# Optimization experiments

Hardware: AMD Instinct MI355X
Metric: run time of the kernel (lower is better)

Reference implementation:

```python
import jax, jax.numpy as jnp
from jax import lax
import numpy as np

B, N, C = 16, 4096, 81          # batch, rois, classes (incl. background)
VARIANCES = np.array([0.1, 0.1, 0.2, 0.2], dtype=np.float32)
MAX_TOTAL = 200                  # max_total_size (= per-class cap here)
K = 200                          # per-class candidates kept before NMS
SCORE_TH = 0.5
IOU_TH = 0.5                     # tf combined NMS default
EPS = 1e-8


def setup_inputs() -> dict:
    key = jax.random.key(0)
    k1, k2, k3, k4 = jax.random.split(key, 4)
    yx = jax.random.uniform(k1, (B, N, 2)) * 0.8
    hw = 0.05 + jax.random.uniform(k2, (B, N, 2)) * 0.15
    roi_bboxes = jnp.concatenate([yx, yx + hw], axis=-1)          # [B,N,4] y1x1y2x2 in [0,1]
    pred_deltas = jax.random.normal(k3, (B, N, C * 4)) * 0.5      # [B,N,C*4]
    logits = jax.random.normal(k4, (B, N, C)) * 3.0
    pred_label_probs = jax.nn.softmax(logits, axis=-1)            # [B,N,C]
    return {"roi_bboxes": roi_bboxes, "pred_deltas": pred_deltas,
            "pred_label_probs": pred_label_probs}


def delta_to_bbox(anchors, deltas):
    # anchors [...,4] y1,x1,y2,x2 ; deltas [...,4] dy,dx,dh,dw
    ah = anchors[..., 2] - anchors[..., 0]
    aw = anchors[..., 3] - anchors[..., 1]
    acy = anchors[..., 0] + 0.5 * ah
    acx = anchors[..., 1] + 0.5 * aw
    bh = jnp.exp(deltas[..., 2]) * ah
    bw = jnp.exp(deltas[..., 3]) * aw
    bcy = deltas[..., 0] * ah + acy
    bcx = deltas[..., 1] * aw + acx
    y1 = bcy - 0.5 * bh
    x1 = bcx - 0.5 * bw
    return jnp.stack([y1, x1, y1 + bh, x1 + bw], axis=-1)


def pairwise_iou(boxes):  # [K,4] -> [K,K]
    y1 = jnp.maximum(boxes[:, None, 0], boxes[None, :, 0])
    x1 = jnp.maximum(boxes[:, None, 1], boxes[None, :, 1])
    y2 = jnp.minimum(boxes[:, None, 2], boxes[None, :, 2])
    x2 = jnp.minimum(boxes[:, None, 3], boxes[None, :, 3])
    inter = jnp.maximum(y2 - y1, 0.0) * jnp.maximum(x2 - x1, 0.0)
    area = jnp.maximum(boxes[:, 2] - boxes[:, 0], 0.0) * jnp.maximum(boxes[:, 3] - boxes[:, 1], 0.0)
    union = area[:, None] + area[None, :] - inter
    return inter / (union + EPS)


def _nms_keep(boxes_k, scores_k):
    # boxes_k [K,4] sorted by score desc; greedy suppression mask
    ious = pairwise_iou(boxes_k)
    rng = jnp.arange(K)
    valid = scores_k > SCORE_TH

    def step(keep, i):
        sup = (ious[i] > IOU_TH) & (rng > i) & keep[i]
        return keep & ~sup, None

    keep, _ = lax.scan(step, valid, rng)
    return keep


def _per_class(boxes_c, scores_c):
    # boxes_c [N,4], scores_c [N] -> top-K candidates + NMS-kept scores
    sc, idx = lax.top_k(scores_c, K)
    bx = boxes_c[idx]                       # [K,4]
    keep = _nms_keep(bx, sc)
    return bx, jnp.where(keep, sc, 0.0)


def _per_image(boxes_b, scores_b):
    # boxes_b [N,C,4], scores_b [N,C]
    bx, sc = jax.vmap(_per_class, in_axes=(1, 1))(boxes_b, scores_b)  # [C,K,4],[C,K]
    top_sc, top_idx = lax.top_k(sc.reshape(-1), MAX_TOTAL)
    top_bx = bx.reshape(-1, 4)[top_idx]
    top_lbl = (top_idx // K).astype(jnp.float32)
    valid = top_sc > 0.0
    top_bx = jnp.clip(jnp.where(valid[:, None], top_bx, 0.0), 0.0, 1.0)  # clip_boxes=True
    return top_bx, jnp.where(valid, top_sc, 0.0), jnp.where(valid, top_lbl, 0.0)


def reference(roi_bboxes, pred_deltas, pred_label_probs):
    b, n, _ = roi_bboxes.shape
    c = pred_label_probs.shape[-1]
    deltas = pred_deltas.reshape(b, n, c, 4) * jnp.asarray(VARIANCES)
    pred_bboxes = delta_to_bbox(roi_bboxes[:, :, None, :], deltas)       # [B,N,C,4]
    bg = jnp.argmax(pred_label_probs, axis=-1) == 0                      # background mask
    scores = jnp.where(bg[..., None], 0.0, pred_label_probs)             # [B,N,C]
    final_bboxes, final_scores, final_labels = jax.vmap(_per_image)(pred_bboxes, scores)
    return final_bboxes, final_labels, final_scores
```

## Files before the change

kernel.cpp:

```cpp
#include <hip/hip_runtime.h>
#include <math.h>

#pragma clang fp contract(off)

constexpr int NB  = 16;
constexpr int NR  = 4096;
constexpr int NC  = 81;
constexpr int KK  = 200;
constexpr int CAP = 4096;
constexpr int SEGCAP = 1024;
constexpr int ROWS_PER_BLK = 64;
constexpr int TCHUNK = 256;
constexpr int NCHUNK = CAP / TCHUNK;
constexpr int OUT_ELEMS = NB * KK * 6;
constexpr float SCORE_TH = 0.5f;
constexpr float IOU_TH   = 0.5f;
constexpr float EPSF     = 1e-8f;

struct Entry {
    float s;
    int   cls;
    int   aux;
    int   pad;
    float y1, x1, y2, x2;
};
static_assert(sizeof(Entry) == 32, "Entry must be 32B");

struct SK { float s; int key; };

__global__ void k_init(int* __restrict__ counts, int* __restrict__ final_count,
                       float* __restrict__ out) {
    int i = blockIdx.x * blockDim.x + threadIdx.x;
    if (i < NB * NC) counts[i] = 0;
    if (i < NB) final_count[i] = 0;
    for (int j = i; j < OUT_ELEMS; j += gridDim.x * blockDim.x) out[j] = 0.f;
}

__global__ void k_classify(const float* __restrict__ roi,
                           const float* __restrict__ deltas,
                           const float* __restrict__ probs,
                           int* __restrict__ counts,
                           Entry* __restrict__ cand) {
    __shared__ float lp[ROWS_PER_BLK * NC];

    const float4* src = (const float4*)(probs + (size_t)blockIdx.x * ROWS_PER_BLK * NC);
    float4* dst = (float4*)lp;
    for (int v = threadIdx.x; v < ROWS_PER_BLK * NC / 4; v += blockDim.x)
        dst[v] = src[v];
    __syncthreads();

    int g = threadIdx.x >> 2;
    int j = threadIdx.x & 3;
    const float* row = lp + g * NC;

    float m = -1.0f;
    int am = 127;
    for (int c = j; c < NC; c += 4) {
        float v = row[c];
        if (v > m) { m = v; am = c; }
    }
    for (int mask = 1; mask <= 2; mask <<= 1) {
        float om = __shfl_xor(m, mask);
        int   oi = __shfl_xor(am, mask);
        if (om > m || (om == m && oi < am)) { m = om; am = oi; }
    }
    if (j != 0) return;
    if (am == 0 || !(m > SCORE_TH)) return;

    int r = blockIdx.x * ROWS_PER_BLK + g;
    int b = r / NR;

    float4 a = ((const float4*)roi)[r];
    float4 d = *(const float4*)(deltas + ((size_t)r * NC + am) * 4);
    float ah  = a.z - a.x;
    float aw  = a.w - a.y;
    float acy = a.x + 0.5f * ah;
    float acx = a.y + 0.5f * aw;
    float dy = d.x * 0.1f, dx = d.y * 0.1f;
    float dh = d.z * 0.2f, dw = d.w * 0.2f;
    float bh  = expf(dh) * ah;
    float bw  = expf(dw) * aw;
    float bcy = dy * ah + acy;
    float bcx = dx * aw + acx;
    float y1 = bcy - 0.5f * bh;
    float x1 = bcx - 0.5f * bw;
    float y2 = y1 + bh;
    float x2 = x1 + bw;

    int slot = atomicAdd(&counts[b * NC + am], 1);
    if (slot < SEGCAP) {
        Entry* e = &cand[(size_t)(b * NC + am) * SEGCAP + slot];
        e->s = m; e->cls = am; e->aux = r % NR; e->pad = 0;
        e->y1 = y1; e->x1 = x1; e->y2 = y2; e->x2 = x2;
    }
}

__global__ void k_perclass(const int* __restrict__ counts,
                           const Entry* __restrict__ cand,
                           int* __restrict__ final_count,
                           Entry* __restrict__ fin,
                           SK* __restrict__ sk) {
    int b = blockIdx.x / NC;
    int c = blockIdx.x % NC;
    if (c == 0) return;
    int Mc = counts[b * NC + c];
    if (Mc > SEGCAP) Mc = SEGCAP;
    if (Mc == 0) return;
    const Entry* seg = cand + (size_t)(b * NC + c) * SEGCAP;

    __shared__ float ls[SEGCAP], ly1[SEGCAP], lx1[SEGCAP], ly2[SEGCAP], lx2[SEGCAP];
    __shared__ int   lroi[SEGCAP];
    __shared__ float ss[KK], sy1[KK], sx1[KK], sy2[KK], sx2[KK], sar[KK];
    __shared__ int   skeep[KK];
    __shared__ int   sbase;

    for (int i = threadIdx.x; i < Mc; i += blockDim.x) {
        Entry e = seg[i];
        ls[i] = e.s; lroi[i] = e.aux;
        ly1[i] = e.y1; lx1[i] = e.x1; ly2[i] = e.y2; lx2[i] = e.x2;
    }
    __syncthreads();

    for (int i = threadIdx.x; i < Mc; i += blockDim.x) {
        float si = ls[i]; int ri = lroi[i];
        int rank = 0;
        for (int j = 0; j < Mc; ++j) {
            float sj = ls[j]; int rj = lroi[j];
            rank += (int)((sj > si) | ((sj == si) & (rj < ri)));
        }
        if (rank < KK) {
            ss[rank] = si;
            sy1[rank] = ly1[i]; sx1[rank] = lx1[i];
            sy2[rank] = ly2[i]; sx2[rank] = lx2[i];
            sar[rank] = fmaxf(ly2[i] - ly1[i], 0.f) * fmaxf(lx2[i] - lx1[i], 0.f);
        }
    }
    __syncthreads();

    int L = Mc < KK ? Mc : KK;
    for (int i = threadIdx.x; i < L; i += blockDim.x) skeep[i] = 1;
    __syncthreads();

    for (int i = 0; i < L; ++i) {
        if (skeep[i]) {
            float yi1 = sy1[i], xi1 = sx1[i], yi2 = sy2[i], xi2 = sx2[i], ai = sar[i];
            for (int j = i + 1 + threadIdx.x; j < L; j += blockDim.x) {
                if (!skeep[j]) continue;
                float yy1 = fmaxf(yi1, sy1[j]), xx1 = fmaxf(xi1, sx1[j]);
                float yy2 = fminf(yi2, sy2[j]), xx2 = fminf(xi2, sx2[j]);
                float inter = fmaxf(yy2 - yy1, 0.f) * fmaxf(xx2 - xx1, 0.f);
                float uni = ai + sar[j] - inter;
                if (inter / (uni + EPSF) > IOU_TH) skeep[j] = 0;
            }
        }
        __syncthreads();
    }

    if (threadIdx.x == 0) {
        int tot = 0;
        for (int i = 0; i < L; ++i) tot += skeep[i];
        sbase = atomicAdd(&final_count[b], tot);
    }
    __syncthreads();
    int base = sbase;

    for (int i = threadIdx.x; i < L; i += blockDim.x) {
        if (skeep[i]) {
            int pos = 0;
            for (int j = 0; j < i; ++j) pos += skeep[j];
            int slot = base + pos;
            if (slot < CAP) {
                Entry* fo = &fin[(size_t)b * CAP + slot];
                fo->s = ss[i]; fo->cls = c; fo->aux = i; fo->pad = 0;
                fo->y1 = sy1[i]; fo->x1 = sx1[i]; fo->y2 = sy2[i]; fo->x2 = sx2[i];
                sk[(size_t)b * CAP + slot].s = ss[i];
                sk[(size_t)b * CAP + slot].key = c * KK + i;
            }
        }
    }
}

__global__ void k_topk(const int* __restrict__ final_count,
                       const Entry* __restrict__ fin,
                       const SK* __restrict__ sk,
                       float* __restrict__ out) {
    int b     = blockIdx.x / NCHUNK;
    int chunk = blockIdx.x % NCHUNK;
    int M = final_count[b];
    if (M > CAP) M = CAP;
    if (chunk * TCHUNK >= M) return;

    __shared__ float sS[CAP];
    __shared__ int   sKy[CAP];
    const SK* list = sk + (size_t)b * CAP;
    for (int i = threadIdx.x; i < M; i += blockDim.x) {
        SK v = list[i];
        sS[i] = v.s; sKy[i] = v.key;
    }
    __syncthreads();

    int e = chunk * TCHUNK + threadIdx.x;
    if (e >= M) return;
    float se = sS[e]; int ke = sKy[e];
    int rank = 0;
    for (int j = 0; j < M; ++j) {
        float sj = sS[j]; int kj = sKy[j];
        rank += (int)((sj > se) | ((sj == se) & (kj < ke)));
    }
    if (rank < KK) {
        Entry en = fin[(size_t)b * CAP + e];
        float* obox = out + (size_t)b * KK * 4;
        float* olbl = out + (size_t)NB * KK * 4 + (size_t)b * KK;
        float* osc  = out + (size_t)NB * KK * 5 + (size_t)b * KK;
        obox[rank * 4 + 0] = fminf(fmaxf(en.y1, 0.f), 1.f);
        obox[rank * 4 + 1] = fminf(fmaxf(en.x1, 0.f), 1.f);
        obox[rank * 4 + 2] = fminf(fmaxf(en.y2, 0.f), 1.f);
        obox[rank * 4 + 3] = fminf(fmaxf(en.x2, 0.f), 1.f);
        olbl[rank] = (float)en.cls;
        osc[rank]  = en.s;
    }
}

extern "C" void kernel_launch(void* const* d_in, const int* in_sizes, int n_in,
                              void* d_out, int out_size, void* d_ws, size_t ws_size,
                              hipStream_t stream) {
    const float* roi    = (const float*)d_in[0];
    const float* deltas = (const float*)d_in[1];
    const float* probs  = (const float*)d_in[2];
    float* out = (float*)d_out;

    int* ws_i        = (int*)d_ws;
    int* counts      = ws_i;
    int* final_count = ws_i + NB * NC;
    Entry* cand = (Entry*)((char*)d_ws + 16384);
    Entry* fin  = cand + (size_t)NB * NC * SEGCAP;
    SK*    sk   = (SK*)(fin + (size_t)NB * CAP);

    k_init<<<80, 256, 0, stream>>>(counts, final_count, out);
    k_classify<<<(NB * NR) / ROWS_PER_BLK, 256, 0, stream>>>(roi, deltas, probs, counts, cand);
    k_perclass<<<NB * NC, 256, 0, stream>>>(counts, cand, final_count, fin, sk);
    k_topk<<<NB * NCHUNK, 256, 0, stream>>>(final_count, fin, sk, out);
}
```

Measured before the change: 84.24 us.

## Run greedy NMS in one wavefront with register keep masks; drop init kernel

The per-class greedy NMS loop now runs on a single 64-lane wavefront. Each lane holds up to four boxes in registers, and the current box is broadcast with shuffles, so the loop no longer needs a block-wide __syncthreads on every iteration. The separate init kernel is replaced by a hipMemsetAsync of the counters, and k_topk chunk 0 zero-fills only the unused output rows. The trade-off is that three quarters of the block sits idle during NMS, and the decode code is refactored into a helper.

```diff
diff --git a/kernel.cpp b/kernel.cpp
--- a/kernel.cpp
+++ b/kernel.cpp
@@ -10,9 +10,9 @@
 constexpr int CAP = 4096;
 constexpr int SEGCAP = 1024;
 constexpr int ROWS_PER_BLK = 64;
+constexpr int GRID = NB * NR / ROWS_PER_BLK;
 constexpr int TCHUNK = 256;
 constexpr int NCHUNK = CAP / TCHUNK;
-constexpr int OUT_ELEMS = NB * KK * 6;
 constexpr float SCORE_TH = 0.5f;
 constexpr float IOU_TH   = 0.5f;
 constexpr float EPSF     = 1e-8f;
@@ -28,50 +28,8 @@
 
 struct SK { float s; int key; };
 
-__global__ void k_init(int* __restrict__ counts, int* __restrict__ final_count,
-                       float* __restrict__ out) {
-    int i = blockIdx.x * blockDim.x + threadIdx.x;
-    if (i < NB * NC) counts[i] = 0;
-    if (i < NB) final_count[i] = 0;
-    for (int j = i; j < OUT_ELEMS; j += gridDim.x * blockDim.x) out[j] = 0.f;
-}
-
-__global__ void k_classify(const float* __restrict__ roi,
-                           const float* __restrict__ deltas,
-                           const float* __restrict__ probs,
-                           int* __restrict__ counts,
-                           Entry* __restrict__ cand) {
-    __shared__ float lp[ROWS_PER_BLK * NC];
-
-    const float4* src = (const float4*)(probs + (size_t)blockIdx.x * ROWS_PER_BLK * NC);
-    float4* dst = (float4*)lp;
-    for (int v = threadIdx.x; v < ROWS_PER_BLK * NC / 4; v += blockDim.x)
-        dst[v] = src[v];
-    __syncthreads();
-
-    int g = threadIdx.x >> 2;
-    int j = threadIdx.x & 3;
-    const float* row = lp + g * NC;
-
-    float m = -1.0f;
-    int am = 127;
-    for (int c = j; c < NC; c += 4) {
-        float v = row[c];
-        if (v > m) { m = v; am = c; }
-    }
-    for (int mask = 1; mask <= 2; mask <<= 1) {
-        float om = __shfl_xor(m, mask);
-        int   oi = __shfl_xor(am, mask);
-        if (om > m || (om == m && oi < am)) { m = om; am = oi; }
-    }
-    if (j != 0) return;
-    if (am == 0 || !(m > SCORE_TH)) return;
-
-    int r = blockIdx.x * ROWS_PER_BLK + g;
-    int b = r / NR;
-
-    float4 a = ((const float4*)roi)[r];
-    float4 d = *(const float4*)(deltas + ((size_t)r * NC + am) * 4);
+__device__ __forceinline__ void decode_box(const float4& a, const float4& d,
+                                           float& y1, float& x1, float& y2, float& x2) {
     float ah  = a.z - a.x;
     float aw  = a.w - a.y;
     float acy = a.x + 0.5f * ah;
@@ -82,11 +40,46 @@
     float bw  = expf(dw) * aw;
     float bcy = dy * ah + acy;
     float bcx = dx * aw + acx;
-    float y1 = bcy - 0.5f * bh;
-    float x1 = bcx - 0.5f * bw;
-    float y2 = y1 + bh;
-    float x2 = x1 + bw;
-
+    y1 = bcy - 0.5f * bh;
+    x1 = bcx - 0.5f * bw;
+    y2 = y1 + bh;
+    x2 = x1 + bw;
+}
+
+__global__ void k_classify(const float* __restrict__ roi,
+                           const float* __restrict__ deltas,
+                           const float* __restrict__ probs,
+                           int* __restrict__ counts,
+                           Entry* __restrict__ cand) {
+    __shared__ float lp[ROWS_PER_BLK * NC];
+    const float4* src = (const float4*)(probs + (size_t)blockIdx.x * ROWS_PER_BLK * NC);
+    float4* dst = (float4*)lp;
+    for (int v = threadIdx.x; v < ROWS_PER_BLK * NC / 4; v += blockDim.x) dst[v] = src[v];
+    __syncthreads();
+
+    int g = threadIdx.x >> 2;
+    int j = threadIdx.x & 3;
+    const float* row = lp + g * NC;
+    float m = -1.0f;
+    int am = 127;
+    for (int c = j; c < NC; c += 4) {
+        float v = row[c];
+        if (v > m) { m = v; am = c; }
+    }
+    for (int mask = 1; mask <= 2; mask <<= 1) {
+        float om = __shfl_xor(m, mask);
+        int   oi = __shfl_xor(am, mask);
+        if (om > m || (om == m && oi < am)) { m = om; am = oi; }
+    }
+    if (j != 0) return;
+    if (am == 0 || !(m > SCORE_TH)) return;
+
+    int r = blockIdx.x * ROWS_PER_BLK + g;
+    int b = r / NR;
+    float4 a = ((const float4*)roi)[r];
+    float4 d = *(const float4*)(deltas + ((size_t)r * NC + am) * 4);
+    float y1, x1, y2, x2;
+    decode_box(a, d, y1, x1, y2, x2);
     int slot = atomicAdd(&counts[b * NC + am], 1);
     if (slot < SEGCAP) {
         Entry* e = &cand[(size_t)(b * NC + am) * SEGCAP + slot];
@@ -100,8 +93,7 @@
                            int* __restrict__ final_count,
                            Entry* __restrict__ fin,
                            SK* __restrict__ sk) {
-    int b = blockIdx.x / NC;
-    int c = blockIdx.x % NC;
+    int b = blockIdx.x / NC, c = blockIdx.x % NC;
     if (c == 0) return;
     int Mc = counts[b * NC + c];
     if (Mc > SEGCAP) Mc = SEGCAP;
@@ -138,23 +130,46 @@
     __syncthreads();
 
     int L = Mc < KK ? Mc : KK;
-    for (int i = threadIdx.x; i < L; i += blockDim.x) skeep[i] = 1;
-    __syncthreads();
-
-    for (int i = 0; i < L; ++i) {
-        if (skeep[i]) {
-            float yi1 = sy1[i], xi1 = sx1[i], yi2 = sy2[i], xi2 = sx2[i], ai = sar[i];
-            for (int j = i + 1 + threadIdx.x; j < L; j += blockDim.x) {
-                if (!skeep[j]) continue;
-                float yy1 = fmaxf(yi1, sy1[j]), xx1 = fmaxf(xi1, sx1[j]);
-                float yy2 = fminf(yi2, sy2[j]), xx2 = fminf(xi2, sx2[j]);
-                float inter = fmaxf(yy2 - yy1, 0.f) * fmaxf(xx2 - xx1, 0.f);
-                float uni = ai + sar[j] - inter;
-                if (inter / (uni + EPSF) > IOU_TH) skeep[j] = 0;
+
+    if (threadIdx.x < 64) {
+        int lane = threadIdx.x;
+        float by1[4], bx1[4], by2[4], bx2[4], bar[4];
+        #pragma unroll
+        for (int s = 0; s < 4; ++s) {
+            int jj = s * 64 + lane;
+            if (jj < L) { by1[s] = sy1[jj]; bx1[s] = sx1[jj]; by2[s] = sy2[jj];
+                          bx2[s] = sx2[jj]; bar[s] = sar[jj]; }
+        }
+        int kmask = 0;
+        #pragma unroll
+        for (int s = 0; s < 4; ++s) if (s * 64 + lane < L) kmask |= 1 << s;
+
+        for (int i = 0; i < L; ++i) {
+            int oi = i & 63, si = i >> 6;
+            int keep_i = (__shfl(kmask, oi) >> si) & 1;
+            if (!keep_i) continue;
+            float yi1 = __shfl(by1[si], oi), xi1 = __shfl(bx1[si], oi);
+            float yi2 = __shfl(by2[si], oi), xi2 = __shfl(bx2[si], oi);
+            float ai  = __shfl(bar[si], oi);
+            #pragma unroll
+            for (int s = 0; s < 4; ++s) {
+                int jj = s * 64 + lane;
+                if (jj > i && jj < L && ((kmask >> s) & 1)) {
+                    float yy1 = fmaxf(yi1, by1[s]), xx1 = fmaxf(xi1, bx1[s]);
+                    float yy2 = fminf(yi2, by2[s]), xx2 = fminf(xi2, bx2[s]);
+                    float inter = fmaxf(yy2 - yy1, 0.f) * fmaxf(xx2 - xx1, 0.f);
+                    float uni = ai + bar[s] - inter;
+                    if (inter / (uni + EPSF) > IOU_TH) kmask &= ~(1 << s);
+                }
             }
         }
-        __syncthreads();
-    }
+        #pragma unroll
+        for (int s = 0; s < 4; ++s) {
+            int jj = s * 64 + lane;
+            if (jj < L) skeep[jj] = (kmask >> s) & 1;
+        }
+    }
+    __syncthreads();
 
     if (threadIdx.x == 0) {
         int tot = 0;
@@ -184,10 +199,22 @@
                        const Entry* __restrict__ fin,
                        const SK* __restrict__ sk,
                        float* __restrict__ out) {
-    int b     = blockIdx.x / NCHUNK;
-    int chunk = blockIdx.x % NCHUNK;
+    int b = blockIdx.x / NCHUNK, chunk = blockIdx.x % NCHUNK;
     int M = final_count[b];
     if (M > CAP) M = CAP;
+
+    float* obox = out + (size_t)b * KK * 4;
+    float* olbl = out + (size_t)NB * KK * 4 + (size_t)b * KK;
+    float* osc  = out + (size_t)NB * KK * 5 + (size_t)b * KK;
+
+    if (chunk == 0) {
+        int Mi = M < KK ? M : KK;
+        for (int i = Mi + (int)threadIdx.x; i < KK; i += blockDim.x) {
+            obox[i * 4 + 0] = 0.f; obox[i * 4 + 1] = 0.f;
+            obox[i * 4 + 2] = 0.f; obox[i * 4 + 3] = 0.f;
+            olbl[i] = 0.f; osc[i] = 0.f;
+        }
+    }
     if (chunk * TCHUNK >= M) return;
 
     __shared__ float sS[CAP];
@@ -209,9 +236,6 @@
     }
     if (rank < KK) {
         Entry en = fin[(size_t)b * CAP + e];
-        float* obox = out + (size_t)b * KK * 4;
-        float* olbl = out + (size_t)NB * KK * 4 + (size_t)b * KK;
-        float* osc  = out + (size_t)NB * KK * 5 + (size_t)b * KK;
         obox[rank * 4 + 0] = fminf(fmaxf(en.y1, 0.f), 1.f);
         obox[rank * 4 + 1] = fminf(fmaxf(en.x1, 0.f), 1.f);
         obox[rank * 4 + 2] = fminf(fmaxf(en.y2, 0.f), 1.f);
@@ -236,8 +260,8 @@
     Entry* fin  = cand + (size_t)NB * NC * SEGCAP;
     SK*    sk   = (SK*)(fin + (size_t)NB * CAP);
 
-    k_init<<<80, 256, 0, stream>>>(counts, final_count, out);
-    k_classify<<<(NB * NR) / ROWS_PER_BLK, 256, 0, stream>>>(roi, deltas, probs, counts, cand);
+    hipMemsetAsync(counts, 0, (NB * NC + NB) * sizeof(int), stream);
+    k_classify<<<GRID, 256, 0, stream>>>(roi, deltas, probs, counts, cand);
     k_perclass<<<NB * NC, 256, 0, stream>>>(counts, cand, final_count, fin, sk);
     k_topk<<<NB * NCHUNK, 256, 0, stream>>>(final_count, fin, sk, out);
 }
```

Measured after the change: 91.21 us. 8.3% more time.
